# Kernel optimization log

Hardware: AMD Instinct MI355X
Metric: run time of the kernel (lower is better)

The kernel has to match this reference:

```python
import jax, jax.numpy as jnp
import numpy as np

N_NODES = 40000
N_EDGES = 640000
IN_SIZE = 128
HIDDEN = 128


def setup_inputs() -> dict:
    key = jax.random.key(0)
    ks = jax.random.split(key, 8)
    x = jax.random.normal(ks[0], (N_NODES, IN_SIZE), dtype=jnp.float32)
    src = jax.random.randint(ks[1], (N_EDGES,), 0, N_NODES, dtype=jnp.int32)
    dst = jax.random.randint(ks[2], (N_EDGES,), 0, N_NODES, dtype=jnp.int32)
    s = 1.0 / np.sqrt(IN_SIZE)
    W_self1 = jax.random.normal(ks[3], (IN_SIZE, HIDDEN), dtype=jnp.float32) * s
    W_neigh1 = jax.random.normal(ks[4], (IN_SIZE, HIDDEN), dtype=jnp.float32) * s
    b1 = jnp.zeros((HIDDEN,), dtype=jnp.float32)
    sh = 1.0 / np.sqrt(HIDDEN)
    W_self2 = jax.random.normal(ks[5], (HIDDEN, HIDDEN), dtype=jnp.float32) * sh
    W_neigh2 = jax.random.normal(ks[6], (HIDDEN, HIDDEN), dtype=jnp.float32) * sh
    b2 = jnp.zeros((HIDDEN,), dtype=jnp.float32)
    return {"x": x, "src": src, "dst": dst,
            "W_self1": W_self1, "W_neigh1": W_neigh1, "b1": b1,
            "W_self2": W_self2, "W_neigh2": W_neigh2, "b2": b2}


def _sage_conv_mean(h, src, dst, W_self, W_neigh, b):
    # gather neighbor (src) features, segment-mean into dst nodes
    gathered = h[src]  # [E, D]
    summed = jax.ops.segment_sum(gathered, dst, num_segments=N_NODES)
    deg = jax.ops.segment_sum(jnp.ones((src.shape[0],), h.dtype), dst,
                              num_segments=N_NODES)
    mean_neigh = summed / jnp.maximum(deg, 1.0)[:, None]
    # DGL SAGEConv 'mean': fc_self(h) + fc_neigh(mean_neigh) + bias
    return h @ W_self + mean_neigh @ W_neigh + b


def reference(x, src, dst, W_self1, W_neigh1, b1, W_self2, W_neigh2, b2):
    h = _sage_conv_mean(x, src, dst, W_self1, W_neigh1, b1)
    h = jax.nn.relu(h)  # relu between layers, not after the last
    h = _sage_conv_mean(h, src, dst, W_self2, W_neigh2, b2)
    return h
```

## Files before the change

kernel.cpp:

```cpp
#include <hip/hip_runtime.h>

#define N_NODES 40000
#define N_EDGES 640000
#define D 128
#define CAP 64
#define ES_CAP (N_NODES * CAP)

typedef __attribute__((ext_vector_type(8))) short short8;
typedef __attribute__((ext_vector_type(4))) float f32x4;
typedef __attribute__((ext_vector_type(2))) float f32x2;

__device__ __forceinline__ unsigned short f2bf(float f) {
    unsigned u = __float_as_uint(f);
    unsigned r = u + 0x7FFF + ((u >> 16) & 1);
    return (unsigned short)(r >> 16);
}


__global__ __launch_bounds__(256) void prep(
    const float* __restrict__ x, unsigned short* __restrict__ xb,
    unsigned short* __restrict__ h1b,
    unsigned char* __restrict__ xq, unsigned char* __restrict__ h1q,
    const float* __restrict__ Ws1, const float* __restrict__ Wn1,
    const float* __restrict__ Ws2, const float* __restrict__ Wn2,
    unsigned* __restrict__ Wp,
    int* __restrict__ cnt, int* __restrict__ edge_src) {
    int t = blockIdx.x * 256 + threadIdx.x;

    if (t < N_NODES) cnt[t] = 0;

    ((int4*)edge_src)[t] = make_int4(N_NODES, N_NODES, N_NODES, N_NODES);

    if (t < 64) {
        ((unsigned*)xb)[N_NODES * 64 + t] = 0;
        ((unsigned*)h1b)[N_NODES * 64 + t] = 0;
    }
    if (t < 32) {
        ((unsigned*)xq)[N_NODES * 32 + t] = 0;
        ((unsigned*)h1q)[N_NODES * 32 + t] = 0;
    }

    {
        float4 a = ((const float4*)x)[t * 2];
        float4 b = ((const float4*)x)[t * 2 + 1];
        uint4 o;
        o.x = f2bf(a.x) | ((unsigned)f2bf(a.y) << 16);
        o.y = f2bf(a.z) | ((unsigned)f2bf(a.w) << 16);
        o.z = f2bf(b.x) | ((unsigned)f2bf(b.y) << 16);
        o.w = f2bf(b.z) | ((unsigned)f2bf(b.w) << 16);
        ((uint4*)xb)[t] = o;
        int p0 = __builtin_amdgcn_cvt_pk_fp8_f32(a.x, a.y, 0, 0);
        p0     = __builtin_amdgcn_cvt_pk_fp8_f32(a.z, a.w, p0, 1);
        int p1 = __builtin_amdgcn_cvt_pk_fp8_f32(b.x, b.y, 0, 0);
        p1     = __builtin_amdgcn_cvt_pk_fp8_f32(b.z, b.w, p1, 1);
        ((uint2*)xq)[t] = make_uint2((unsigned)p0, (unsigned)p1);
    }

    if (t < 32768) {
        int L   = t >> 14;
        int rem = t & 16383;
        int j2 = rem & 3;
        int l  = (rem >> 2) & 63;
        int c  = (rem >> 8) & 7;
        int q  = rem >> 11;
        const float* W = (L == 0) ? (q < 4 ? Ws1 : Wn1) : (q < 4 ? Ws2 : Wn2);
        int k0  = (q & 3) * 32 + (l >> 4) * 8 + 2 * j2;
        int col = c * 16 + (l & 15);
        float v0 = W[(size_t)k0 * D + col];
        float v1 = W[(size_t)(k0 + 1) * D + col];
        Wp[t] = f2bf(v0) | ((unsigned)f2bf(v1) << 16);
    }
}


__global__ void fill_edges(const int* __restrict__ src, const int* __restrict__ dst,
                           int* __restrict__ cnt, int* __restrict__ edge_src) {
    int e = blockIdx.x * 256 + threadIdx.x;
    if (e < N_EDGES) {
        int d = dst[e];
        int p = atomicAdd(&cnt[d], 1);
        if (p < CAP) edge_src[d * CAP + p] = src[e];
    }
}


#define PADW 68

__global__ __launch_bounds__(512) void fused_layer(
    const unsigned short* __restrict__ A,
    const unsigned char* __restrict__ Aq,
    const int* __restrict__ deg,
    const int* __restrict__ edge_src,
    const unsigned* __restrict__ Wp,
    const float* __restrict__ bias,
    unsigned short* __restrict__ outb,
    unsigned char*  __restrict__ outq,
    float* __restrict__ outf,
    int do_relu) {
    __shared__ float sf[32 * 132];
    unsigned* meanL = (unsigned*)sf;

    int tid = threadIdx.x;
    int w = tid >> 6, l = tid & 63;
    int blk = blockIdx.x;
    int grp = l >> 4, sub = l & 15;

    {
        int myn = blk * 32 + w * 4 + grp;
        int dgv = deg[myn];
        int e   = myn * CAP;
        int pd  = (dgv + 15) & ~15;
        if (pd > CAP) pd = CAP;
        int end = e + pd;
        const uint2* q8 = (const uint2*)Aq;
        f32x2 ca = {0.f, 0.f}, cb = {0.f, 0.f}, cc = {0.f, 0.f}, cd = {0.f, 0.f};
        for (; e < end; e += 8) {
            int4 qa = *(const int4*)&edge_src[e];
            int4 qb = *(const int4*)&edge_src[e + 4];
            uint2 u0 = q8[(size_t)qa.x * 16 + sub];
            uint2 u1 = q8[(size_t)qa.y * 16 + sub];
            uint2 u2 = q8[(size_t)qa.z * 16 + sub];
            uint2 u3 = q8[(size_t)qa.w * 16 + sub];
            uint2 u4 = q8[(size_t)qb.x * 16 + sub];
            uint2 u5 = q8[(size_t)qb.y * 16 + sub];
            uint2 u6 = q8[(size_t)qb.z * 16 + sub];
            uint2 u7 = q8[(size_t)qb.w * 16 + sub];
            ca += __builtin_amdgcn_cvt_pk_f32_fp8((int)u0.x, 0);
            cb += __builtin_amdgcn_cvt_pk_f32_fp8((int)u0.x, 1);
            cc += __builtin_amdgcn_cvt_pk_f32_fp8((int)u0.y, 0);
            cd += __builtin_amdgcn_cvt_pk_f32_fp8((int)u0.y, 1);
            ca += __builtin_amdgcn_cvt_pk_f32_fp8((int)u1.x, 0);
            cb += __builtin_amdgcn_cvt_pk_f32_fp8((int)u1.x, 1);
            cc += __builtin_amdgcn_cvt_pk_f32_fp8((int)u1.y, 0);
            cd += __builtin_amdgcn_cvt_pk_f32_fp8((int)u1.y, 1);
            ca += __builtin_amdgcn_cvt_pk_f32_fp8((int)u2.x, 0);
            cb += __builtin_amdgcn_cvt_pk_f32_fp8((int)u2.x, 1);
            cc += __builtin_amdgcn_cvt_pk_f32_fp8((int)u2.y, 0);
            cd += __builtin_amdgcn_cvt_pk_f32_fp8((int)u2.y, 1);
            ca += __builtin_amdgcn_cvt_pk_f32_fp8((int)u3.x, 0);
            cb += __builtin_amdgcn_cvt_pk_f32_fp8((int)u3.x, 1);
            cc += __builtin_amdgcn_cvt_pk_f32_fp8((int)u3.y, 0);
            cd += __builtin_amdgcn_cvt_pk_f32_fp8((int)u3.y, 1);
            ca += __builtin_amdgcn_cvt_pk_f32_fp8((int)u4.x, 0);
            cb += __builtin_amdgcn_cvt_pk_f32_fp8((int)u4.x, 1);
            cc += __builtin_amdgcn_cvt_pk_f32_fp8((int)u4.y, 0);
            cd += __builtin_amdgcn_cvt_pk_f32_fp8((int)u4.y, 1);
            ca += __builtin_amdgcn_cvt_pk_f32_fp8((int)u5.x, 0);
            cb += __builtin_amdgcn_cvt_pk_f32_fp8((int)u5.x, 1);
            cc += __builtin_amdgcn_cvt_pk_f32_fp8((int)u5.y, 0);
            cd += __builtin_amdgcn_cvt_pk_f32_fp8((int)u5.y, 1);
            ca += __builtin_amdgcn_cvt_pk_f32_fp8((int)u6.x, 0);
            cb += __builtin_amdgcn_cvt_pk_f32_fp8((int)u6.x, 1);
            cc += __builtin_amdgcn_cvt_pk_f32_fp8((int)u6.y, 0);
            cd += __builtin_amdgcn_cvt_pk_f32_fp8((int)u6.y, 1);
            ca += __builtin_amdgcn_cvt_pk_f32_fp8((int)u7.x, 0);
            cb += __builtin_amdgcn_cvt_pk_f32_fp8((int)u7.x, 1);
            cc += __builtin_amdgcn_cvt_pk_f32_fp8((int)u7.y, 0);
            cd += __builtin_amdgcn_cvt_pk_f32_fp8((int)u7.y, 1);
        }
        float inv = dgv > 0 ? 1.0f / (float)dgv : 0.f;
        uint4 o;
        o.x = f2bf(ca.x * inv) | ((unsigned)f2bf(ca.y * inv) << 16);
        o.y = f2bf(cb.x * inv) | ((unsigned)f2bf(cb.y * inv) << 16);
        o.z = f2bf(cc.x * inv) | ((unsigned)f2bf(cc.y * inv) << 16);
        o.w = f2bf(cd.x * inv) | ((unsigned)f2bf(cd.y * inv) << 16);
        *(uint4*)&meanL[(w * 4 + grp) * PADW + sub * 4] = o;
    }

    int rlo = l & 15, khi = l >> 4;
    int row0g = blk * 32 + (w >> 2) * 16;
    const unsigned short* ar = A + (size_t)(row0g + rlo) * D + khi * 8;

    f32x4 acc[2] = {};
    #pragma unroll
    for (int q = 0; q < 4; ++q) {
        short8 a = *(const short8*)(ar + q * 32);
        #pragma unroll
        for (int c = 0; c < 2; ++c) {
            int cg = (w & 3) * 2 + c;
            short8 b = *(const short8*)(Wp + ((q * 8 + cg) * 64 + l) * 4);
            acc[c] = __builtin_amdgcn_mfma_f32_16x16x32_bf16(a, b, acc[c], 0, 0, 0);
        }
    }
    __syncthreads();
    int lr0 = (w >> 2) * 16 + rlo;
    #pragma unroll
    for (int q = 4; q < 8; ++q) {
        short8 a = *(const short8*)(meanL + lr0 * PADW + khi * 4 + (q & 3) * 16);
        #pragma unroll
        for (int c = 0; c < 2; ++c) {
            int cg = (w & 3) * 2 + c;
            short8 b = *(const short8*)(Wp + ((q * 8 + cg) * 64 + l) * 4);
            acc[c] = __builtin_amdgcn_mfma_f32_16x16x32_bf16(a, b, acc[c], 0, 0, 0);
        }
    }
    __syncthreads();

    #pragma unroll
    for (int c = 0; c < 2; ++c) {
        int cg = (w & 3) * 2 + c;
        #pragma unroll
        for (int j = 0; j < 4; ++j)
            sf[((w >> 2) * 16 + khi * 4 + j) * 132 + cg * 16 + rlo] = acc[c][j];
    }
    __syncthreads();

    int row = tid >> 4, c0 = (tid & 15) * 8;
    const float* srow = &sf[row * 132 + c0];
    float4 u0 = *(const float4*)(srow + 0);
    float4 u1 = *(const float4*)(srow + 4);
    float4 b0 = *(const float4*)(bias + c0 + 0);
    float4 b1 = *(const float4*)(bias + c0 + 4);
    size_t grow = (size_t)blk * 32 + row;
    if (do_relu) {
        float f0 = fmaxf(u0.x + b0.x, 0.f), f1 = fmaxf(u0.y + b0.y, 0.f);
        float f2 = fmaxf(u0.z + b0.z, 0.f), f3 = fmaxf(u0.w + b0.w, 0.f);
        float f4 = fmaxf(u1.x + b1.x, 0.f), f5 = fmaxf(u1.y + b1.y, 0.f);
        float f6 = fmaxf(u1.z + b1.z, 0.f), f7 = fmaxf(u1.w + b1.w, 0.f);
        uint4 o;
        o.x = f2bf(f0) | ((unsigned)f2bf(f1) << 16);
        o.y = f2bf(f2) | ((unsigned)f2bf(f3) << 16);
        o.z = f2bf(f4) | ((unsigned)f2bf(f5) << 16);
        o.w = f2bf(f6) | ((unsigned)f2bf(f7) << 16);
        *(uint4*)(outb + grow * D + c0) = o;
        int pq0 = __builtin_amdgcn_cvt_pk_fp8_f32(f0, f1, 0, 0);
        pq0     = __builtin_amdgcn_cvt_pk_fp8_f32(f2, f3, pq0, 1);
        int pq1 = __builtin_amdgcn_cvt_pk_fp8_f32(f4, f5, 0, 0);
        pq1     = __builtin_amdgcn_cvt_pk_fp8_f32(f6, f7, pq1, 1);
        *(uint2*)(outq + grow * D + c0) = make_uint2((unsigned)pq0, (unsigned)pq1);
    } else {
        float4 o0 = {u0.x + b0.x, u0.y + b0.y, u0.z + b0.z, u0.w + b0.w};
        float4 o1 = {u1.x + b1.x, u1.y + b1.y, u1.z + b1.z, u1.w + b1.w};
        *(float4*)(outf + grow * D + c0 + 0) = o0;
        *(float4*)(outf + grow * D + c0 + 4) = o1;
    }
}


extern "C" void kernel_launch(void* const* d_in, const int* in_sizes, int n_in,
                              void* d_out, int out_size, void* d_ws, size_t ws_size,
                              hipStream_t stream) {
    const float* x       = (const float*)d_in[0];
    const int*   src     = (const int*)d_in[1];
    const int*   dst     = (const int*)d_in[2];
    const float* W_self1 = (const float*)d_in[3];
    const float* W_neigh1= (const float*)d_in[4];
    const float* b1      = (const float*)d_in[5];
    const float* W_self2 = (const float*)d_in[6];
    const float* W_neigh2= (const float*)d_in[7];
    const float* b2      = (const float*)d_in[8];
    float* out = (float*)d_out;

    char* ws = (char*)d_ws;
    size_t off_cnt  = 0;
    size_t off_es   = 160256;
    size_t off_xb   = 10400512;
    size_t off_h1b  = 20640768;
    size_t off_wp   = 30881024;
    size_t off_xq   = 31012096;
    size_t off_h1q  = 36132224;
    size_t total    = 41252352;
    if (ws_size < total) return;

    int* cnt       = (int*)(ws + off_cnt);
    int* edge_src  = (int*)(ws + off_es);
    unsigned short* xb   = (unsigned short*)(ws + off_xb);
    unsigned short* h1b  = (unsigned short*)(ws + off_h1b);
    unsigned* Wp         = (unsigned*)(ws + off_wp);
    unsigned char* xq    = (unsigned char*)(ws + off_xq);
    unsigned char* h1q   = (unsigned char*)(ws + off_h1q);

    prep<<<2500, 256, 0, stream>>>(x, xb, h1b, xq, h1q,
                                   W_self1, W_neigh1, W_self2, W_neigh2,
                                   Wp, cnt, edge_src);
    fill_edges<<<(N_EDGES + 255) / 256, 256, 0, stream>>>(src, dst, cnt, edge_src);

    fused_layer<<<N_NODES / 32, 512, 0, stream>>>(xb, xq, cnt, edge_src,
                                                  Wp, b1, h1b, h1q, nullptr, 1);
    fused_layer<<<N_NODES / 32, 512, 0, stream>>>(h1b, h1q, cnt, edge_src,
                                                  Wp + 16384, b2, nullptr, nullptr,
                                                  out, 0);
}
```

Measured before the change: 96.78 us.

## Merge all stages into one cooperative persistent kernel with grid syncs

Replaces the four launches (prep, edge fill, two layers) with a single cooperative kernel that uses grid-wide syncs between stages and atomic tile stealing for the layer phases. The 10 MB edge_src sentinel fill is removed; the gather now masks slots past the degree to the zero padding row, and padding is rounded to 8 instead of 16. The aim is to cut launch gaps and write traffic. In exchange it adds grid-sync barriers, tile-counter atomics, and an occupancy-limited grid. A multi-kernel fallback runs if the cooperative launch fails.

New measurement: 227.1 us. 2.35x slower.

```diff
diff --git a/kernel.cpp b/kernel.cpp
--- a/kernel.cpp
+++ b/kernel.cpp
@@ -1,10 +1,14 @@
 #include <hip/hip_runtime.h>
+#include <hip/hip_cooperative_groups.h>
+
+namespace cg = cooperative_groups;
 
 #define N_NODES 40000
 #define N_EDGES 640000
 #define D 128
 #define CAP 64
 #define ES_CAP (N_NODES * CAP)
+#define NTILES (N_NODES / 32)
 
 typedef __attribute__((ext_vector_type(8))) short short8;
 typedef __attribute__((ext_vector_type(4))) float f32x4;
@@ -17,29 +21,18 @@
 }
 
 
-__global__ __launch_bounds__(256) void prep(
-    const float* __restrict__ x, unsigned short* __restrict__ xb,
-    unsigned short* __restrict__ h1b,
+__device__ __forceinline__ void prep_work(
+    int t, const float* __restrict__ x, unsigned short* __restrict__ xb,
     unsigned char* __restrict__ xq, unsigned char* __restrict__ h1q,
     const float* __restrict__ Ws1, const float* __restrict__ Wn1,
     const float* __restrict__ Ws2, const float* __restrict__ Wn2,
-    unsigned* __restrict__ Wp,
-    int* __restrict__ cnt, int* __restrict__ edge_src) {
-    int t = blockIdx.x * 256 + threadIdx.x;
-
+    unsigned* __restrict__ Wp, int* __restrict__ cnt, int* __restrict__ tctr) {
     if (t < N_NODES) cnt[t] = 0;
-
-    ((int4*)edge_src)[t] = make_int4(N_NODES, N_NODES, N_NODES, N_NODES);
-
-    if (t < 64) {
-        ((unsigned*)xb)[N_NODES * 64 + t] = 0;
-        ((unsigned*)h1b)[N_NODES * 64 + t] = 0;
-    }
+    if (t < 2) tctr[t] = 0;
     if (t < 32) {
         ((unsigned*)xq)[N_NODES * 32 + t] = 0;
         ((unsigned*)h1q)[N_NODES * 32 + t] = 0;
     }
-
     {
         float4 a = ((const float4*)x)[t * 2];
         float4 b = ((const float4*)x)[t * 2 + 1];
@@ -55,7 +48,6 @@
         p1     = __builtin_amdgcn_cvt_pk_fp8_f32(b.z, b.w, p1, 1);
         ((uint2*)xq)[t] = make_uint2((unsigned)p0, (unsigned)p1);
     }
-
     if (t < 32768) {
         int L   = t >> 14;
         int rem = t & 16383;
@@ -72,59 +64,56 @@
     }
 }
 
-
-__global__ void fill_edges(const int* __restrict__ src, const int* __restrict__ dst,
-                           int* __restrict__ cnt, int* __restrict__ edge_src) {
-    int e = blockIdx.x * 256 + threadIdx.x;
-    if (e < N_EDGES) {
-        int d = dst[e];
-        int p = atomicAdd(&cnt[d], 1);
-        if (p < CAP) edge_src[d * CAP + p] = src[e];
-    }
+__device__ __forceinline__ void fill_work(
+    int e, const int* __restrict__ src, const int* __restrict__ dst,
+    int* __restrict__ cnt, int* __restrict__ edge_src) {
+    int d = dst[e];
+    int p = atomicAdd(&cnt[d], 1);
+    if (p < CAP) edge_src[d * CAP + p] = src[e];
 }
 
 
 #define PADW 68
 
-__global__ __launch_bounds__(512) void fused_layer(
-    const unsigned short* __restrict__ A,
+__device__ __forceinline__ void layer_tile(
+    int blk, const unsigned short* __restrict__ A,
     const unsigned char* __restrict__ Aq,
-    const int* __restrict__ deg,
-    const int* __restrict__ edge_src,
-    const unsigned* __restrict__ Wp,
-    const float* __restrict__ bias,
-    unsigned short* __restrict__ outb,
-    unsigned char*  __restrict__ outq,
-    float* __restrict__ outf,
-    int do_relu) {
-    __shared__ float sf[32 * 132];
+    const int* __restrict__ deg, const int* __restrict__ edge_src,
+    const unsigned* __restrict__ Wp, const float* __restrict__ bias,
+    unsigned short* __restrict__ outb, unsigned char* __restrict__ outq,
+    float* __restrict__ outf, int do_relu, float* sf) {
     unsigned* meanL = (unsigned*)sf;
-
     int tid = threadIdx.x;
     int w = tid >> 6, l = tid & 63;
-    int blk = blockIdx.x;
     int grp = l >> 4, sub = l & 15;
 
     {
         int myn = blk * 32 + w * 4 + grp;
         int dgv = deg[myn];
-        int e   = myn * CAP;
-        int pd  = (dgv + 15) & ~15;
+        int base = myn * CAP;
+        int pd = (dgv + 7) & ~7;
         if (pd > CAP) pd = CAP;
-        int end = e + pd;
         const uint2* q8 = (const uint2*)Aq;
         f32x2 ca = {0.f, 0.f}, cb = {0.f, 0.f}, cc = {0.f, 0.f}, cd = {0.f, 0.f};
-        for (; e < end; e += 8) {
-            int4 qa = *(const int4*)&edge_src[e];
-            int4 qb = *(const int4*)&edge_src[e + 4];
-            uint2 u0 = q8[(size_t)qa.x * 16 + sub];
-            uint2 u1 = q8[(size_t)qa.y * 16 + sub];
-            uint2 u2 = q8[(size_t)qa.z * 16 + sub];
-            uint2 u3 = q8[(size_t)qa.w * 16 + sub];
-            uint2 u4 = q8[(size_t)qb.x * 16 + sub];
-            uint2 u5 = q8[(size_t)qb.y * 16 + sub];
-            uint2 u6 = q8[(size_t)qb.z * 16 + sub];
-            uint2 u7 = q8[(size_t)qb.w * 16 + sub];
+        for (int s = 0; s < pd; s += 8) {
+            int4 qa = *(const int4*)&edge_src[base + s];
+            int4 qb = *(const int4*)&edge_src[base + s + 4];
+            int i0 = (s + 0 < dgv) ? qa.x : N_NODES;
+            int i1 = (s + 1 < dgv) ? qa.y : N_NODES;
+            int i2 = (s + 2 < dgv) ? qa.z : N_NODES;
+            int i3 = (s + 3 < dgv) ? qa.w : N_NODES;
+            int i4 = (s + 4 < dgv) ? qb.x : N_NODES;
+            int i5 = (s + 5 < dgv) ? qb.y : N_NODES;
+            int i6 = (s + 6 < dgv) ? qb.z : N_NODES;
+            int i7 = (s + 7 < dgv) ? qb.w : N_NODES;
+            uint2 u0 = q8[(size_t)i0 * 16 + sub];
+            uint2 u1 = q8[(size_t)i1 * 16 + sub];
+            uint2 u2 = q8[(size_t)i2 * 16 + sub];
+            uint2 u3 = q8[(size_t)i3 * 16 + sub];
+            uint2 u4 = q8[(size_t)i4 * 16 + sub];
+            uint2 u5 = q8[(size_t)i5 * 16 + sub];
+            uint2 u6 = q8[(size_t)i6 * 16 + sub];
+            uint2 u7 = q8[(size_t)i7 * 16 + sub];
             ca += __builtin_amdgcn_cvt_pk_f32_fp8((int)u0.x, 0);
             cb += __builtin_amdgcn_cvt_pk_f32_fp8((int)u0.x, 1);
             cc += __builtin_amdgcn_cvt_pk_f32_fp8((int)u0.y, 0);
@@ -237,19 +226,92 @@
 }
 
 
+__global__ __launch_bounds__(512) void mega(
+    const float* __restrict__ x, const int* __restrict__ src,
+    const int* __restrict__ dst,
+    const float* __restrict__ Ws1, const float* __restrict__ Wn1,
+    const float* __restrict__ b1,
+    const float* __restrict__ Ws2, const float* __restrict__ Wn2,
+    const float* __restrict__ b2,
+    unsigned short* __restrict__ xb, unsigned short* __restrict__ h1b,
+    unsigned char* __restrict__ xq, unsigned char* __restrict__ h1q,
+    unsigned* __restrict__ Wp, int* __restrict__ cnt,
+    int* __restrict__ edge_src, int* __restrict__ tctr,
+    float* __restrict__ out) {
+    cg::grid_group gg = cg::this_grid();
+    __shared__ float sf[32 * 132];
+    __shared__ int stile;
+    int g0 = blockIdx.x * 512 + threadIdx.x;
+    int gsz = gridDim.x * 512;
+
+    for (int t = g0; t < 640000; t += gsz)
+        prep_work(t, x, xb, xq, h1q, Ws1, Wn1, Ws2, Wn2, Wp, cnt, tctr);
+    gg.sync();
+    for (int e = g0; e < N_EDGES; e += gsz)
+        fill_work(e, src, dst, cnt, edge_src);
+    gg.sync();
+    for (;;) {
+        __syncthreads();
+        if (threadIdx.x == 0) stile = atomicAdd(&tctr[0], 1);
+        __syncthreads();
+        int tile = stile;
+        if (tile >= NTILES) break;
+        layer_tile(tile, xb, xq, cnt, edge_src, Wp, b1, h1b, h1q, nullptr, 1, sf);
+    }
+    gg.sync();
+    for (;;) {
+        __syncthreads();
+        if (threadIdx.x == 0) stile = atomicAdd(&tctr[1], 1);
+        __syncthreads();
+        int tile = stile;
+        if (tile >= NTILES) break;
+        layer_tile(tile, h1b, h1q, cnt, edge_src, Wp + 16384, b2, nullptr, nullptr,
+                   out, 0, sf);
+    }
+}
+
+
+__global__ __launch_bounds__(256) void prep_k(
+    const float* __restrict__ x, unsigned short* __restrict__ xb,
+    unsigned char* __restrict__ xq, unsigned char* __restrict__ h1q,
+    const float* __restrict__ Ws1, const float* __restrict__ Wn1,
+    const float* __restrict__ Ws2, const float* __restrict__ Wn2,
+    unsigned* __restrict__ Wp, int* __restrict__ cnt, int* __restrict__ tctr) {
+    int t = blockIdx.x * 256 + threadIdx.x;
+    prep_work(t, x, xb, xq, h1q, Ws1, Wn1, Ws2, Wn2, Wp, cnt, tctr);
+}
+
+__global__ void fill_k(const int* __restrict__ src, const int* __restrict__ dst,
+                       int* __restrict__ cnt, int* __restrict__ edge_src) {
+    int e = blockIdx.x * 256 + threadIdx.x;
+    if (e < N_EDGES) fill_work(e, src, dst, cnt, edge_src);
+}
+
+__global__ __launch_bounds__(512) void fused_k(
+    const unsigned short* __restrict__ A, const unsigned char* __restrict__ Aq,
+    const int* __restrict__ deg, const int* __restrict__ edge_src,
+    const unsigned* __restrict__ Wp, const float* __restrict__ bias,
+    unsigned short* __restrict__ outb, unsigned char* __restrict__ outq,
+    float* __restrict__ outf, int do_relu) {
+    __shared__ float sf[32 * 132];
+    layer_tile(blockIdx.x, A, Aq, deg, edge_src, Wp, bias, outb, outq, outf,
+               do_relu, sf);
+}
+
+
 extern "C" void kernel_launch(void* const* d_in, const int* in_sizes, int n_in,
                               void* d_out, int out_size, void* d_ws, size_t ws_size,
                               hipStream_t stream) {
     const float* x       = (const float*)d_in[0];
     const int*   src     = (const int*)d_in[1];
     const int*   dst     = (const int*)d_in[2];
-    const float* W_self1 = (const float*)d_in[3];
-    const float* W_neigh1= (const float*)d_in[4];
+    const float* Ws1     = (const float*)d_in[3];
+    const float* Wn1     = (const float*)d_in[4];
     const float* b1      = (const float*)d_in[5];
-    const float* W_self2 = (const float*)d_in[6];
-    const float* W_neigh2= (const float*)d_in[7];
+    const float* Ws2     = (const float*)d_in[6];
+    const float* Wn2     = (const float*)d_in[7];
     const float* b2      = (const float*)d_in[8];
-    float* out = (float*)d_out;
+    float* outp = (float*)d_out;
 
     char* ws = (char*)d_ws;
     size_t off_cnt  = 0;
@@ -259,7 +321,8 @@
     size_t off_wp   = 30881024;
     size_t off_xq   = 31012096;
     size_t off_h1q  = 36132224;
-    size_t total    = 41252352;
+    size_t off_tc   = 41252352;
+    size_t total    = 41252608;
     if (ws_size < total) return;
 
     int* cnt       = (int*)(ws + off_cnt);
@@ -269,15 +332,32 @@
     unsigned* Wp         = (unsigned*)(ws + off_wp);
     unsigned char* xq    = (unsigned char*)(ws + off_xq);
     unsigned char* h1q   = (unsigned char*)(ws + off_h1q);
-
-    prep<<<2500, 256, 0, stream>>>(x, xb, h1b, xq, h1q,
-                                   W_self1, W_neigh1, W_self2, W_neigh2,
-                                   Wp, cnt, edge_src);
-    fill_edges<<<(N_EDGES + 255) / 256, 256, 0, stream>>>(src, dst, cnt, edge_src);
-
-    fused_layer<<<N_NODES / 32, 512, 0, stream>>>(xb, xq, cnt, edge_src,
-                                                  Wp, b1, h1b, h1q, nullptr, 1);
-    fused_layer<<<N_NODES / 32, 512, 0, stream>>>(h1b, h1q, cnt, edge_src,
-                                                  Wp + 16384, b2, nullptr, nullptr,
-                                                  out, 0);
-}
+    int* tctr            = (int*)(ws + off_tc);
+
+    int maxB = 0;
+    hipError_t qe = hipOccupancyMaxActiveBlocksPerMultiprocessor(&maxB, mega, 512, 0);
+    int grid = (qe == hipSuccess && maxB > 0) ? maxB * 256 : 0;
+    if (grid > NTILES) grid = NTILES;
+
+    bool coop_ok = false;
+    if (grid >= 256) {
+        void* args[] = {(void*)&x, (void*)&src, (void*)&dst,
+                        (void*)&Ws1, (void*)&Wn1, (void*)&b1,
+                        (void*)&Ws2, (void*)&Wn2, (void*)&b2,
+                        (void*)&xb, (void*)&h1b, (void*)&xq, (void*)&h1q,
+                        (void*)&Wp, (void*)&cnt, (void*)&edge_src,
+                        (void*)&tctr, (void*)&outp};
+        hipError_t le = hipLaunchCooperativeKernel(mega, dim3(grid), dim3(512),
+                                                   args, 0, stream);
+        coop_ok = (le == hipSuccess);
+    }
+    if (!coop_ok) {
+        prep_k<<<2500, 256, 0, stream>>>(x, xb, xq, h1q, Ws1, Wn1, Ws2, Wn2,
+                                         Wp, cnt, tctr);
+        fill_k<<<2500, 256, 0, stream>>>(src, dst, cnt, edge_src);
+        fused_k<<<NTILES, 512, 0, stream>>>(xb, xq, cnt, edge_src, Wp, b1,
+                                            h1b, h1q, nullptr, 1);
+        fused_k<<<NTILES, 512, 0, stream>>>(h1b, h1q, cnt, edge_src, Wp + 16384,
+                                            b2, nullptr, nullptr, outp, 0);
+    }
+}
```
